# Kernel tuning notes

Measured on AMD Instinct MI355X. Metric: run time of the kernel, lower is better.

Reference implementation:

```python
import jax, jax.numpy as jnp
from jax import lax
import numpy as np

T, B, D, H = 4096, 32, 512, 256


def setup_inputs() -> dict:
    key = jax.random.key(0)
    ks = jax.random.split(key, 8)
    s_ih = 1.0 / np.sqrt(H)
    inp = {
        "x": jax.random.normal(ks[0], (T, B, D), dtype=jnp.float32),
        "reset": jax.random.randint(ks[1], (T, B), 0, 2, dtype=jnp.int32),
        # PyTorch nn.LSTM params, gate order (i, f, g, o)
        "W_ih": jax.random.uniform(ks[2], (4 * H, D), jnp.float32, -s_ih, s_ih),
        "W_hh": jax.random.uniform(ks[3], (4 * H, H), jnp.float32, -s_ih, s_ih),
        "b_ih": jax.random.uniform(ks[4], (4 * H,), jnp.float32, -s_ih, s_ih),
        "b_hh": jax.random.uniform(ks[5], (4 * H,), jnp.float32, -s_ih, s_ih),
        "W_proj": jax.random.uniform(ks[6], (1, H), jnp.float32, -s_ih, s_ih),
        "b_proj": jax.random.uniform(ks[7], (1,), jnp.float32, -s_ih, s_ih),
    }
    return inp


def _lstm_with_reset(x, reset, W_ih, W_hh, b_ih, b_hh):
    # Precompute input contribution for all timesteps: [T, B, 4H]
    xW = jnp.einsum("tbd,gd->tbg", x, W_ih) + b_ih + b_hh
    h0 = jnp.zeros((x.shape[1], H), x.dtype)
    c0 = jnp.zeros((x.shape[1], H), x.dtype)

    def step(carry, inp):
        h, c = carry
        xw, r = inp
        keep = (1 - r).astype(h.dtype)[:, None]  # zero state at episode starts
        h = h * keep
        c = c * keep
        gates = xw + h @ W_hh.T  # [B, 4H]
        i, f, g, o = jnp.split(gates, 4, axis=-1)
        c = jax.nn.sigmoid(f) * c + jax.nn.sigmoid(i) * jnp.tanh(g)
        h = jax.nn.sigmoid(o) * jnp.tanh(c)
        return (h, c), h

    (_, _), hs = lax.scan(step, (h0, c0), (xW, reset))
    return hs  # [T, B, H]


def reference(x, reset, W_ih, W_hh, b_ih, b_hh, W_proj, b_proj):
    hs = _lstm_with_reset(x, reset, W_ih, W_hh, b_ih, b_hh)
    return hs @ W_proj.T + b_proj  # [T, B, 1]
```

## Files before the change

kernel.cpp:

```cpp
#include <hip/hip_runtime.h>
#include <cstdint>
#include <cstddef>

#define T_DIM 4096
#define B_DIM 32
#define D_DIM 512
#define H_DIM 256
#define G_DIM 1024
#define HSTR 264
#define NBUCK 64

typedef _Float16 h8 __attribute__((ext_vector_type(8)));
typedef float f4 __attribute__((ext_vector_type(4)));

__global__ void seg_build_kernel(const int* __restrict__ reset,
                                 unsigned* __restrict__ starts,
                                 unsigned* __restrict__ segcnt) {
  __shared__ unsigned cnts[256];
  __shared__ unsigned offs[256];
  const int b = blockIdx.x;
  const int tid = threadIdx.x;
  const int t0 = tid * 16;
  unsigned c = 0;
  for (int e = 0; e < 16; ++e) {
    int t = t0 + e;
    bool pred = (t == 0) || (reset[t * B_DIM + b] != 0);
    c += pred ? 1u : 0u;
  }
  cnts[tid] = c;
  __syncthreads();
  if (tid == 0) {
    unsigned run = 0;
    for (int i = 0; i < 256; ++i) { unsigned v = cnts[i]; offs[i] = run; run += v; }
    segcnt[b] = run;
  }
  __syncthreads();
  unsigned o = (unsigned)b * 4096u + offs[tid];
  for (int e = 0; e < 16; ++e) {
    int t = t0 + e;
    bool pred = (t == 0) || (reset[t * B_DIM + b] != 0);
    if (pred) { starts[o++] = (unsigned)t; }
  }
}

__global__ void seg_flat_kernel(const unsigned* __restrict__ starts,
                                const unsigned* __restrict__ segcnt,
                                uint2* __restrict__ flat2,
                                unsigned* __restrict__ meta) {
  __shared__ unsigned offs;
  const int b = blockIdx.x;
  const int tid = threadIdx.x;
  if (tid == 0) {
    unsigned o = 0;
    for (int i = 0; i < b; ++i) o += segcnt[i];
    offs = o;
    if (b == 31) meta[1] = o + segcnt[31];
    if (b == 0) meta[0] = 0u;
  }
  __syncthreads();
  const unsigned cnt = segcnt[b];
  const unsigned off = offs;
  for (unsigned s = tid; s < cnt; s += 256) {
    unsigned t0 = starts[b * 4096u + s];
    unsigned t1 = (s + 1 < cnt) ? starts[b * 4096u + s + 1] : 4096u;
    flat2[off + s] = make_uint2(t0 | ((unsigned)b << 16), t1);
  }
}

__global__ void seg_sort_kernel(const uint2* __restrict__ flat2,
                                uint2* __restrict__ flat,
                                const unsigned* __restrict__ meta) {
  __shared__ unsigned lh[NBUCK];
  __shared__ unsigned cur[NBUCK];
  const unsigned nseg = meta[1];
  const int tid = threadIdx.x;
  const int lane = tid & 63;
  if (tid < NBUCK) lh[tid] = 0u;
  __syncthreads();
  for (unsigned base = 0; base < nseg; base += 1024) {
    unsigned i = base + tid;
    bool act = i < nseg;
    unsigned bk = 0u;
    if (act) {
      uint2 e = flat2[i];
      bk = min(e.y - (e.x & 0xFFFFu), (unsigned)NBUCK) - 1u;
    }
    unsigned long long rem = __ballot(act);
    while (rem) {
      int ld = (int)__ffsll((unsigned long long)rem) - 1;
      unsigned lbk = __shfl(bk, ld);
      unsigned long long meq = __ballot(act && bk == lbk);
      if (lane == ld) atomicAdd(&lh[lbk], (unsigned)__popcll(meq));
      rem &= ~meq;
    }
  }
  __syncthreads();
  if (tid == 0) {
    unsigned run = 0;
    for (int k = NBUCK - 1; k >= 0; --k) { cur[k] = run; run += lh[k]; }
  }
  __syncthreads();
  for (unsigned base = 0; base < nseg; base += 1024) {
    unsigned i = base + tid;
    bool act = i < nseg;
    uint2 e = make_uint2(0u, 0u);
    unsigned bk = 0u;
    if (act) {
      e = flat2[i];
      bk = min(e.y - (e.x & 0xFFFFu), (unsigned)NBUCK) - 1u;
    }
    unsigned long long rem = __ballot(act);
    unsigned pos = 0u;
    while (rem) {
      int ld = (int)__ffsll((unsigned long long)rem) - 1;
      unsigned lbk = __shfl(bk, ld);
      unsigned long long meq = __ballot(act && bk == lbk);
      unsigned bs = 0u;
      if (lane == ld) bs = atomicAdd(&cur[lbk], (unsigned)__popcll(meq));
      bs = __shfl(bs, ld);
      if (act && bk == lbk)
        pos = bs + (unsigned)__popcll(meq & ((1ull << lane) - 1ull));
      rem &= ~meq;
    }
    if (act) flat[pos] = e;
  }
}

__global__ void wpack_kernel(const float* __restrict__ Whh,
                             _Float16* __restrict__ wpack) {
  int gid = blockIdx.x * 256 + threadIdx.x;
  int nt = gid >> 9;
  int rem = gid & 511;
  int ks = rem >> 6;
  int l = rem & 63;
  int n = nt * 16 + (l & 15);
  int k = ks * 32 + (l >> 4) * 8;
  const float* src = Whh + (size_t)n * H_DIM + k;
  f4 v0 = *(const f4*)src;
  f4 v1 = *(const f4*)(src + 4);
  h8 wv = {(_Float16)v0.x, (_Float16)v0.y, (_Float16)v0.z, (_Float16)v0.w,
           (_Float16)v1.x, (_Float16)v1.y, (_Float16)v1.z, (_Float16)v1.w};
  *(h8*)(wpack + (size_t)gid * 8) = wv;
}

#define BM 128
#define BN 128
#define BK 32

__global__ __launch_bounds__(256) void xw_gemm_kernel(
    const float* __restrict__ X, const float* __restrict__ Wih,
    const float* __restrict__ bih, const float* __restrict__ bhh,
    _Float16* __restrict__ xw) {
  __shared__ _Float16 As[BM * BK];
  __shared__ _Float16 Bs[BN * BK];
  const int tid = threadIdx.x;
  const int lane = tid & 63;
  const int wave = tid >> 6;
  const unsigned wg = blockIdx.x;
  const unsigned xcd = wg & 7u;
  const unsigned idx = wg >> 3;
  const size_t m0 = (size_t)(xcd * 128u + (idx >> 3)) * BM;
  const int n0 = (int)(idx & 7u) * BN;
  const int wm = (wave & 1) * 64;
  const int wn = (wave >> 1) * 64;
  const int q = lane >> 4;
  const int r = lane & 15;

  f4 acc[4][4];
#pragma unroll
  for (int i = 0; i < 4; ++i)
#pragma unroll
    for (int j = 0; j < 4; ++j) { f4 z = {0.f, 0.f, 0.f, 0.f}; acc[i][j] = z; }

  const int srow = tid >> 1;
  const int kh = (tid & 1) * 16;

  for (int k0 = 0; k0 < D_DIM; k0 += BK) {
    const float* ax = X + (m0 + (size_t)srow) * D_DIM + k0 + kh;
    const float* bx = Wih + ((size_t)(n0 + srow)) * D_DIM + k0 + kh;
    f4 a0 = *(const f4*)(ax);
    f4 a1 = *(const f4*)(ax + 4);
    f4 a2 = *(const f4*)(ax + 8);
    f4 a3 = *(const f4*)(ax + 12);
    f4 b0 = *(const f4*)(bx);
    f4 b1 = *(const f4*)(bx + 4);
    f4 b2 = *(const f4*)(bx + 8);
    f4 b3 = *(const f4*)(bx + 12);
    h8 ha0 = {(_Float16)a0.x, (_Float16)a0.y, (_Float16)a0.z, (_Float16)a0.w,
              (_Float16)a1.x, (_Float16)a1.y, (_Float16)a1.z, (_Float16)a1.w};
    h8 ha1 = {(_Float16)a2.x, (_Float16)a2.y, (_Float16)a2.z, (_Float16)a2.w,
              (_Float16)a3.x, (_Float16)a3.y, (_Float16)a3.z, (_Float16)a3.w};
    h8 hb0 = {(_Float16)b0.x, (_Float16)b0.y, (_Float16)b0.z, (_Float16)b0.w,
              (_Float16)b1.x, (_Float16)b1.y, (_Float16)b1.z, (_Float16)b1.w};
    h8 hb1 = {(_Float16)b2.x, (_Float16)b2.y, (_Float16)b2.z, (_Float16)b2.w,
              (_Float16)b3.x, (_Float16)b3.y, (_Float16)b3.z, (_Float16)b3.w};
    *(h8*)(As + srow * BK + kh) = ha0;
    *(h8*)(As + srow * BK + kh + 8) = ha1;
    *(h8*)(Bs + srow * BK + kh) = hb0;
    *(h8*)(Bs + srow * BK + kh + 8) = hb1;
    __syncthreads();

    h8 af[4], bf[4];
#pragma unroll
    for (int mi = 0; mi < 4; ++mi)
      af[mi] = *(const h8*)(As + (wm + mi * 16 + r) * BK + q * 8);
#pragma unroll
    for (int ni = 0; ni < 4; ++ni)
      bf[ni] = *(const h8*)(Bs + (wn + ni * 16 + r) * BK + q * 8);
#pragma unroll
    for (int mi = 0; mi < 4; ++mi)
#pragma unroll
      for (int ni = 0; ni < 4; ++ni)
        acc[mi][ni] = __builtin_amdgcn_mfma_f32_16x16x32_f16(af[mi], bf[ni], acc[mi][ni], 0, 0, 0);
    __syncthreads();
  }

#pragma unroll
  for (int mi = 0; mi < 4; ++mi) {
#pragma unroll
    for (int ni = 0; ni < 4; ++ni) {
      int n = n0 + wn + ni * 16 + r;
      float bias = bih[n] + bhh[n];
#pragma unroll
      for (int reg = 0; reg < 4; ++reg) {
        size_t m = m0 + (size_t)(wm + mi * 16 + q * 4 + reg);
        __builtin_nontemporal_store((_Float16)(acc[mi][ni][reg] + bias),
                                    &xw[m * G_DIM + n]);
      }
    }
  }
}

__device__ __forceinline__ float sigmf(float x) {
  return __builtin_amdgcn_rcpf(1.f + __expf(-x));
}
__device__ __forceinline__ float tanhf_(float x) {
  return 2.f * __builtin_amdgcn_rcpf(1.f + __expf(-2.f * x)) - 1.f;
}
__device__ __forceinline__ f4 MF(h8 a, h8 b, f4 c) {
  return __builtin_amdgcn_mfma_f32_16x16x32_f16(a, b, c, 0, 0, 0);
}

#define WPKp(g, j, ks) \
  ((const h8*)(wpack + (((size_t)((((g)*16 + 2*w + (j)) * 8 + (ks))) * 64 + l) * 8)))
#define WLDp(g, j, ks2) \
  (*(const h8*)(Wlds + ((((ks2)*64) + ((g)*16 + 2*w + (j))) * 64 + l) * 8))
#define ARD(mt, ks) (*(const h8*)(Hbuf + (16*(mt) + r16) * HSTR + (ks)*32 + q*8))

#define MFK_REG(KS) do {                                                   \
  h8 a0_ = ARD(0, KS), a1_ = ARD(1, KS);                                   \
  _Pragma("unroll") for (int g = 0; g < 4; ++g)                            \
  _Pragma("unroll") for (int j = 0; j < 2; ++j) {                          \
    acc[0][g][j] = MF(a0_, wr[g][j][KS], acc[0][g][j]);                    \
    acc[1][g][j] = MF(a1_, wr[g][j][KS], acc[1][g][j]); }                  \
} while (0)

#define MFK_LDS(KS2, KS) do {                                              \
  h8 a0_ = ARD(0, KS), a1_ = ARD(1, KS);                                   \
  _Pragma("unroll") for (int g = 0; g < 4; ++g)                            \
  _Pragma("unroll") for (int j = 0; j < 2; ++j) {                          \
    h8 b_ = WLDp(g, j, KS2);                                               \
    acc[0][g][j] = MF(a0_, b_, acc[0][g][j]);                              \
    acc[1][g][j] = MF(a1_, b_, acc[1][g][j]); }                            \
} while (0)

#define MFK_STR(KS) do {                                                   \
  h8 a0_ = ARD(0, KS), a1_ = ARD(1, KS);                                   \
  _Pragma("unroll") for (int g = 0; g < 4; ++g)                            \
  _Pragma("unroll") for (int j = 0; j < 2; ++j) {                          \
    acc[0][g][j] = MF(a0_, sreg[g][j], acc[0][g][j]);                      \
    acc[1][g][j] = MF(a1_, sreg[g][j], acc[1][g][j]); }                    \
} while (0)

#define LOAD_STR(KS) do {                                                  \
  _Pragma("unroll") for (int g = 0; g < 4; ++g)                            \
  _Pragma("unroll") for (int j = 0; j < 2; ++j)                            \
    sreg[g][j] = *WPKp(g, j, KS);                                          \
} while (0)

#define XWG(MT, G, J, RB, NB) do {                                         \
  f4 xv;                                                                   \
  xv.x = (float)__builtin_nontemporal_load(                                \
      (const _Float16*)(xwc + RB.x + (G)*512 + (NB)));                     \
  xv.y = (float)__builtin_nontemporal_load(                                \
      (const _Float16*)(xwc + RB.y + (G)*512 + (NB)));                     \
  xv.z = (float)__builtin_nontemporal_load(                                \
      (const _Float16*)(xwc + RB.z + (G)*512 + (NB)));                     \
  xv.w = (float)__builtin_nontemporal_load(                                \
      (const _Float16*)(xwc + RB.w + (G)*512 + (NB)));                     \
  acc[MT][G][J] += xv; } while (0)

#define CONTROL_STEP do {                                                    \
  int m = tid;                                                               \
  if (alivef[m]) {                                                           \
    unsigned oi = outix[m];                                                  \
    if (oi != 0xFFFFFFFFu) {                                                 \
      float s = bp;                                                          \
      _Pragma("unroll") for (int ww = 0; ww < 8; ++ww) s += pbuf[ww][m];     \
      __builtin_nontemporal_store(s, &out[oi]);                              \
    }                                                                        \
    int t = tcur[m] + 1;                                                     \
    if (t < tend[m]) {                                                       \
      tcur[m] = t; keepm[m] = 1.f;                                           \
      unsigned row = (unsigned)t * 32u + (unsigned)bcol[m];                  \
      trowB[m] = row * 2048u; outix[m] = row;                                \
    } else {                                                                 \
      unsigned idx = atomicAdd(ctr, 1u);                                     \
      if (idx < nseg) {                                                      \
        uint2 sg = flat[idx];                                                \
        int t0s = (int)(sg.x & 0xFFFFu); int bb = (int)(sg.x >> 16);         \
        tcur[m] = t0s; tend[m] = (int)sg.y; bcol[m] = bb; keepm[m] = 0.f;    \
        unsigned row = (unsigned)t0s * 32u + (unsigned)bb;                   \
        trowB[m] = row * 2048u; outix[m] = row;                              \
        h8 zz = {0,0,0,0,0,0,0,0};                                           \
        _Pragma("unroll") for (int i2 = 0; i2 < 33; ++i2)                    \
          *(h8*)(Hbuf + (size_t)m * HSTR + i2 * 8) = zz;                     \
      } else {                                                               \
        alivef[m] = 0; outix[m] = 0xFFFFFFFFu; trowB[m] = 0;                 \
        keepm[m] = 0.f;                                                      \
      }                                                                      \
    }                                                                        \
  }                                                                          \
} while (0)

__global__ __launch_bounds__(512, 2) void lstm_scan_mfma(
    const _Float16* __restrict__ xw,
    const _Float16* __restrict__ wpack,
    const float* __restrict__ Wproj,
    const float* __restrict__ bproj,
    const uint2* __restrict__ flat,
    unsigned* __restrict__ meta,
    float* __restrict__ out) {
  __shared__ __align__(16) _Float16 Wlds[2 * 64 * 64 * 8];
  __shared__ __align__(16) _Float16 Hbuf[32 * HSTR];
  __shared__ __align__(16) float pbuf[8][32];
  __shared__ __align__(16) unsigned trowB[32];
  __shared__ __align__(16) float keepm[32];
  __shared__ unsigned outix[32];
  __shared__ int tcur[32], tend[32], bcol[32], alivef[32];

  const int tid = threadIdx.x;
  const int l = tid & 63;
  const int w = tid >> 6;
  const int q = l >> 4;
  const int r16 = l & 15;
  const char* xwc = (const char*)xw;
  unsigned* ctr = meta;
  const unsigned nseg = meta[1];

  for (int it = 0; it < 16; ++it) {
    int idx = it * 512 + tid;
    int ks2 = idx >> 12;
    int nt = (idx >> 6) & 63;
    int ll = idx & 63;
    *(h8*)(Wlds + (size_t)idx * 8) =
        *(const h8*)(wpack + (((size_t)(nt * 8 + ks2 + 4)) * 64 + ll) * 8);
  }
  for (int i = tid; i < 32 * HSTR / 8; i += 512) {
    h8 z = {0,0,0,0,0,0,0,0};
    *(h8*)(Hbuf + (size_t)i * 8) = z;
  }
  h8 wr[4][2][4];
#pragma unroll
  for (int g = 0; g < 4; ++g)
#pragma unroll
    for (int j = 0; j < 2; ++j)
#pragma unroll
      for (int ks = 0; ks < 4; ++ks)
        wr[g][j][ks] = *WPKp(g, j, ks);

  const float wpv0 = Wproj[32 * w + r16];
  const float wpv1 = Wproj[32 * w + 16 + r16];
  const float bp = bproj[0];
  if (tid < 32) {
    alivef[tid] = 1; tcur[tid] = 0; tend[tid] = 0; bcol[tid] = 0;
    outix[tid] = 0xFFFFFFFFu; trowB[tid] = 0; keepm[tid] = 0.f;
  }
  float cst[16];
#pragma unroll
  for (int i = 0; i < 16; ++i) cst[i] = 0.f;
  __syncthreads();
  if (tid < 32) CONTROL_STEP;
  int nalive = __syncthreads_count(tid < 32 ? alivef[tid] : 0);

  while (nalive > 0) {
    f4 z4 = {0.f, 0.f, 0.f, 0.f};
    f4 acc[2][4][2];
#pragma unroll
    for (int mt = 0; mt < 2; ++mt)
#pragma unroll
      for (int g = 0; g < 4; ++g)
#pragma unroll
        for (int j = 0; j < 2; ++j) acc[mt][g][j] = z4;
    h8 sreg[4][2];

    LOAD_STR(6);
    MFK_REG(0);
    MFK_STR(6);
    LOAD_STR(7);
    MFK_REG(1);
    MFK_STR(7);
    MFK_REG(2);
    MFK_REG(3);
    MFK_LDS(0, 4);
    MFK_LDS(1, 5);

    __syncthreads();

    uint4 rb0 = *(const uint4*)&trowB[q * 4];
    uint4 rb1 = *(const uint4*)&trowB[16 + q * 4];
    const int nb0 = w * 64 + r16 * 2;
    const int nb1 = nb0 + 32;
    XWG(0, 0, 0, rb0, nb0); XWG(0, 0, 1, rb0, nb1);
    XWG(0, 1, 0, rb0, nb0); XWG(0, 1, 1, rb0, nb1);
    XWG(0, 2, 0, rb0, nb0); XWG(0, 2, 1, rb0, nb1);
    XWG(0, 3, 0, rb0, nb0); XWG(0, 3, 1, rb0, nb1);
    XWG(1, 0, 0, rb1, nb0); XWG(1, 0, 1, rb1, nb1);
    XWG(1, 1, 0, rb1, nb0); XWG(1, 1, 1, rb1, nb1);
    XWG(1, 2, 0, rb1, nb0); XWG(1, 2, 1, rb1, nb1);
    XWG(1, 3, 0, rb1, nb0); XWG(1, 3, 1, rb1, nb1);

    f4 kp0 = *(const f4*)&keepm[q * 4];
    f4 kp1 = *(const f4*)&keepm[16 + q * 4];
    float pr[8];
#pragma unroll
    for (int r = 0; r < 4; ++r) {
      {
        float gi = sigmf(acc[0][0][0][r]);
        float gf = sigmf(acc[0][1][0][r]);
        float gg = tanhf_(acc[0][2][0][r]);
        float go = sigmf(acc[0][3][0][r]);
        float cn = gf * (cst[r] * kp0[r]) + gi * gg;
        cst[r] = cn;
        float hv = go * tanhf_(cn);
        Hbuf[(q * 4 + r) * HSTR + 32 * w + r16] = (_Float16)hv;
        pr[r] = hv * wpv0;
      }
      {
        float gi = sigmf(acc[0][0][1][r]);
        float gf = sigmf(acc[0][1][1][r]);
        float gg = tanhf_(acc[0][2][1][r]);
        float go = sigmf(acc[0][3][1][r]);
        float cn = gf * (cst[4 + r] * kp0[r]) + gi * gg;
        cst[4 + r] = cn;
        float hv = go * tanhf_(cn);
        Hbuf[(q * 4 + r) * HSTR + 32 * w + 16 + r16] = (_Float16)hv;
        pr[r] += hv * wpv1;
      }
    }
#pragma unroll
    for (int r = 0; r < 4; ++r) {
      {
        float gi = sigmf(acc[1][0][0][r]);
        float gf = sigmf(acc[1][1][0][r]);
        float gg = tanhf_(acc[1][2][0][r]);
        float go = sigmf(acc[1][3][0][r]);
        float cn = gf * (cst[8 + r] * kp1[r]) + gi * gg;
        cst[8 + r] = cn;
        float hv = go * tanhf_(cn);
        Hbuf[(16 + q * 4 + r) * HSTR + 32 * w + r16] = (_Float16)hv;
        pr[4 + r] = hv * wpv0;
      }
      {
        float gi = sigmf(acc[1][0][1][r]);
        float gf = sigmf(acc[1][1][1][r]);
        float gg = tanhf_(acc[1][2][1][r]);
        float go = sigmf(acc[1][3][1][r]);
        float cn = gf * (cst[12 + r] * kp1[r]) + gi * gg;
        cst[12 + r] = cn;
        float hv = go * tanhf_(cn);
        Hbuf[(16 + q * 4 + r) * HSTR + 32 * w + 16 + r16] = (_Float16)hv;
        pr[4 + r] += hv * wpv1;
      }
    }
#pragma unroll
    for (int jj = 0; jj < 8; ++jj) {
      pr[jj] += __shfl_xor(pr[jj], 1);
      pr[jj] += __shfl_xor(pr[jj], 2);
      pr[jj] += __shfl_xor(pr[jj], 4);
      pr[jj] += __shfl_xor(pr[jj], 8);
    }
    if (r16 == 0) {
#pragma unroll
      for (int jj = 0; jj < 8; ++jj)
        pbuf[w][16 * (jj >> 2) + q * 4 + (jj & 3)] = pr[jj];
    }

    __syncthreads();
    if (tid < 32) CONTROL_STEP;
    nalive = __syncthreads_count(tid < 32 ? alivef[tid] : 0);
  }
}

extern "C" void kernel_launch(void* const* d_in, const int* in_sizes, int n_in,
                              void* d_out, int out_size, void* d_ws, size_t ws_size,
                              hipStream_t stream) {
  const float* x = (const float*)d_in[0];
  const int* reset = (const int*)d_in[1];
  const float* Wih = (const float*)d_in[2];
  const float* Whh = (const float*)d_in[3];
  const float* bih = (const float*)d_in[4];
  const float* bhh = (const float*)d_in[5];
  const float* Wproj = (const float*)d_in[6];
  const float* bproj = (const float*)d_in[7];
  float* out = (float*)d_out;

  char* ws = (char*)d_ws;
  _Float16* xw = (_Float16*)ws;
  unsigned* starts = (unsigned*)(ws + 268435456ULL);
  unsigned* segcnt = (unsigned*)(ws + 268959744ULL);
  uint2* flat = (uint2*)(ws + 268959872ULL);
  _Float16* wpack = (_Float16*)(ws + 270008448ULL);
  unsigned* meta = (unsigned*)(ws + 270532736ULL);
  uint2* flat2 = (uint2*)ws;

  hipLaunchKernelGGL(seg_build_kernel, dim3(32), dim3(256), 0, stream,
                     reset, starts, segcnt);
  hipLaunchKernelGGL(seg_flat_kernel, dim3(32), dim3(256), 0, stream,
                     starts, segcnt, flat2, meta);
  hipLaunchKernelGGL(seg_sort_kernel, dim3(1), dim3(1024), 0, stream,
                     flat2, flat, meta);
  hipLaunchKernelGGL(wpack_kernel, dim3(128), dim3(256), 0, stream,
                     Whh, wpack);
  hipLaunchKernelGGL(xw_gemm_kernel, dim3(8192), dim3(256), 0, stream,
                     x, Wih, bih, bhh, xw);
  hipLaunchKernelGGL(lstm_scan_mfma, dim3(256), dim3(512), 0, stream,
                     xw, wpack, Wproj, bproj, flat, meta, out);
}
```

Measured before the change: 1.276 ms.

## Stage xW rows into LDS via async global_load_lds and rebalance W_hh placement

At the start of each recurrent step, the 32 rows of precomputed input gates are prefetched into an LDS buffer with async global-to-LDS loads, which overlap the recurrent MFMA work. Previously each lane issued many scattered nontemporal fp16 global loads after the barrier. The W_hh k-slices are redistributed: fewer are held in registers, one is held in LDS, and the rest are streamed from global memory through double-buffered registers. The segment-claim atomic is aggregated per wavefront with a ballot, and the GEMM store becomes a normal store so xW stays in cache. The cost is extra LDS, which may limit occupancy, and more global weight traffic per step.

```diff
diff --git a/kernel.cpp b/kernel.cpp
--- a/kernel.cpp
+++ b/kernel.cpp
@@ -8,6 +8,7 @@
 #define H_DIM 256
 #define G_DIM 1024
 #define HSTR 264
+#define XSTR 1036
 #define NBUCK 64
 
 typedef _Float16 h8 __attribute__((ext_vector_type(8)));
@@ -224,8 +225,7 @@
 #pragma unroll
       for (int reg = 0; reg < 4; ++reg) {
         size_t m = m0 + (size_t)(wm + mi * 16 + q * 4 + reg);
-        __builtin_nontemporal_store((_Float16)(acc[mi][ni][reg] + bias),
-                                    &xw[m * G_DIM + n]);
+        xw[m * G_DIM + n] = (_Float16)(acc[mi][ni][reg] + bias);
       }
     }
   }
@@ -243,8 +243,6 @@
 
 #define WPKp(g, j, ks) \
   ((const h8*)(wpack + (((size_t)((((g)*16 + 2*w + (j)) * 8 + (ks))) * 64 + l) * 8)))
-#define WLDp(g, j, ks2) \
-  (*(const h8*)(Wlds + ((((ks2)*64) + ((g)*16 + 2*w + (j))) * 64 + l) * 8))
 #define ARD(mt, ks) (*(const h8*)(Hbuf + (16*(mt) + r16) * HSTR + (ks)*32 + q*8))
 
 #define MFK_REG(KS) do {                                                   \
@@ -255,72 +253,83 @@
     acc[1][g][j] = MF(a1_, wr[g][j][KS], acc[1][g][j]); }                  \
 } while (0)
 
-#define MFK_LDS(KS2, KS) do {                                              \
+#define MFK_W2() do {                                                      \
+  h8 a0_ = ARD(0, 2), a1_ = ARD(1, 2);                                     \
+  _Pragma("unroll") for (int g = 0; g < 4; ++g)                            \
+  _Pragma("unroll") for (int j = 0; j < 2; ++j) {                          \
+    h8 b_ = *(const h8*)(Wlds + (size_t)((((g)*16 + 2*w + (j)) * 64 + l)) * 8); \
+    acc[0][g][j] = MF(a0_, b_, acc[0][g][j]);                              \
+    acc[1][g][j] = MF(a1_, b_, acc[1][g][j]); }                            \
+} while (0)
+
+#define MFK_S(BUF, KS) do {                                                \
   h8 a0_ = ARD(0, KS), a1_ = ARD(1, KS);                                   \
   _Pragma("unroll") for (int g = 0; g < 4; ++g)                            \
   _Pragma("unroll") for (int j = 0; j < 2; ++j) {                          \
-    h8 b_ = WLDp(g, j, KS2);                                               \
-    acc[0][g][j] = MF(a0_, b_, acc[0][g][j]);                              \
-    acc[1][g][j] = MF(a1_, b_, acc[1][g][j]); }                            \
+    acc[0][g][j] = MF(a0_, BUF[g][j], acc[0][g][j]);                       \
+    acc[1][g][j] = MF(a1_, BUF[g][j], acc[1][g][j]); }                     \
 } while (0)
 
-#define MFK_STR(KS) do {                                                   \
-  h8 a0_ = ARD(0, KS), a1_ = ARD(1, KS);                                   \
-  _Pragma("unroll") for (int g = 0; g < 4; ++g)                            \
-  _Pragma("unroll") for (int j = 0; j < 2; ++j) {                          \
-    acc[0][g][j] = MF(a0_, sreg[g][j], acc[0][g][j]);                      \
-    acc[1][g][j] = MF(a1_, sreg[g][j], acc[1][g][j]); }                    \
-} while (0)
-
-#define LOAD_STR(KS) do {                                                  \
+#define LOAD_S(BUF, KS) do {                                               \
   _Pragma("unroll") for (int g = 0; g < 4; ++g)                            \
   _Pragma("unroll") for (int j = 0; j < 2; ++j)                            \
-    sreg[g][j] = *WPKp(g, j, KS);                                          \
+    BUF[g][j] = *WPKp(g, j, KS);                                           \
 } while (0)
 
-#define XWG(MT, G, J, RB, NB) do {                                         \
+#define XRD(MT, G, J) do {                                                 \
   f4 xv;                                                                   \
-  xv.x = (float)__builtin_nontemporal_load(                                \
-      (const _Float16*)(xwc + RB.x + (G)*512 + (NB)));                     \
-  xv.y = (float)__builtin_nontemporal_load(                                \
-      (const _Float16*)(xwc + RB.y + (G)*512 + (NB)));                     \
-  xv.z = (float)__builtin_nontemporal_load(                                \
-      (const _Float16*)(xwc + RB.z + (G)*512 + (NB)));                     \
-  xv.w = (float)__builtin_nontemporal_load(                                \
-      (const _Float16*)(xwc + RB.w + (G)*512 + (NB)));                     \
+  int rb_ = 16*(MT) + q*4;                                                 \
+  int nn_ = (G)*256 + w*32 + 16*(J) + r16;                                 \
+  xv.x = (float)xwlds[(rb_+0)*XSTR + nn_];                                 \
+  xv.y = (float)xwlds[(rb_+1)*XSTR + nn_];                                 \
+  xv.z = (float)xwlds[(rb_+2)*XSTR + nn_];                                 \
+  xv.w = (float)xwlds[(rb_+3)*XSTR + nn_];                                 \
   acc[MT][G][J] += xv; } while (0)
 
-#define CONTROL_STEP do {                                                    \
-  int m = tid;                                                               \
-  if (alivef[m]) {                                                           \
-    unsigned oi = outix[m];                                                  \
-    if (oi != 0xFFFFFFFFu) {                                                 \
-      float s = bp;                                                          \
-      _Pragma("unroll") for (int ww = 0; ww < 8; ++ww) s += pbuf[ww][m];     \
-      __builtin_nontemporal_store(s, &out[oi]);                              \
-    }                                                                        \
-    int t = tcur[m] + 1;                                                     \
-    if (t < tend[m]) {                                                       \
-      tcur[m] = t; keepm[m] = 1.f;                                           \
-      unsigned row = (unsigned)t * 32u + (unsigned)bcol[m];                  \
-      trowB[m] = row * 2048u; outix[m] = row;                                \
-    } else {                                                                 \
-      unsigned idx = atomicAdd(ctr, 1u);                                     \
-      if (idx < nseg) {                                                      \
-        uint2 sg = flat[idx];                                                \
-        int t0s = (int)(sg.x & 0xFFFFu); int bb = (int)(sg.x >> 16);         \
-        tcur[m] = t0s; tend[m] = (int)sg.y; bcol[m] = bb; keepm[m] = 0.f;    \
-        unsigned row = (unsigned)t0s * 32u + (unsigned)bb;                   \
-        trowB[m] = row * 2048u; outix[m] = row;                              \
-        h8 zz = {0,0,0,0,0,0,0,0};                                           \
-        _Pragma("unroll") for (int i2 = 0; i2 < 33; ++i2)                    \
-          *(h8*)(Hbuf + (size_t)m * HSTR + i2 * 8) = zz;                     \
-      } else {                                                               \
-        alivef[m] = 0; outix[m] = 0xFFFFFFFFu; trowB[m] = 0;                 \
-        keepm[m] = 0.f;                                                      \
-      }                                                                      \
-    }                                                                        \
-  }                                                                          \
+#define CONTROL_STEP do {                                                     \
+  int m = tid;                                                                \
+  bool aliv = alivef[m] != 0;                                                 \
+  if (aliv) {                                                                 \
+    unsigned oi = outix[m];                                                   \
+    if (oi != 0xFFFFFFFFu) {                                                  \
+      float s = bp;                                                           \
+      _Pragma("unroll") for (int ww = 0; ww < 8; ++ww) s += pbuf[ww][m];      \
+      __builtin_nontemporal_store(s, &out[oi]);                               \
+    }                                                                         \
+  }                                                                           \
+  bool cont = aliv && (tcur[m] + 1 < tend[m]);                                \
+  bool need = aliv && !cont;                                                  \
+  unsigned long long bal = __ballot(need);                                    \
+  if (cont) {                                                                 \
+    int t = tcur[m] + 1;                                                      \
+    tcur[m] = t; keepm[m] = 1.f;                                              \
+    unsigned row = (unsigned)t * 32u + (unsigned)bcol[m];                     \
+    trowB[m] = row * 2048u; outix[m] = row;                                   \
+  }                                                                           \
+  if (bal) {                                                                  \
+    unsigned cntp = (unsigned)__popcll(bal);                                  \
+    int ldr = (int)__ffsll(bal) - 1;                                          \
+    unsigned basep = 0;                                                       \
+    if ((tid & 63) == ldr) basep = atomicAdd(ctr, cntp);                      \
+    basep = __shfl(basep, ldr);                                               \
+    if (need) {                                                               \
+      unsigned idx = basep +                                                  \
+          (unsigned)__popcll(bal & ((1ull << (tid & 63)) - 1ull));            \
+      if (idx < nseg) {                                                       \
+        uint2 sg = flat[idx];                                                 \
+        int t0s = (int)(sg.x & 0xFFFFu); int bb = (int)(sg.x >> 16);          \
+        tcur[m] = t0s; tend[m] = (int)sg.y; bcol[m] = bb; keepm[m] = 0.f;     \
+        unsigned row = (unsigned)t0s * 32u + (unsigned)bb;                    \
+        trowB[m] = row * 2048u; outix[m] = row;                               \
+        h8 zz = {0,0,0,0,0,0,0,0};                                            \
+        _Pragma("unroll") for (int i2 = 0; i2 < 33; ++i2)                     \
+          *(h8*)(Hbuf + (size_t)m * HSTR + i2 * 8) = zz;                      \
+      } else {                                                                \
+        alivef[m] = 0; outix[m] = 0xFFFFFFFFu; trowB[m] = 0;                  \
+        keepm[m] = 0.f;                                                       \
+      }                                                                       \
+    }                                                                         \
+  }                                                                           \
 } while (0)
 
 __global__ __launch_bounds__(512, 2) void lstm_scan_mfma(
@@ -331,7 +340,8 @@
     const uint2* __restrict__ flat,
     unsigned* __restrict__ meta,
     float* __restrict__ out) {
-  __shared__ __align__(16) _Float16 Wlds[2 * 64 * 64 * 8];
+  __shared__ __align__(16) _Float16 Wlds[64 * 64 * 8];
+  __shared__ __align__(16) _Float16 xwlds[32 * XSTR];
   __shared__ __align__(16) _Float16 Hbuf[32 * HSTR];
   __shared__ __align__(16) float pbuf[8][32];
   __shared__ __align__(16) unsigned trowB[32];
@@ -350,23 +360,22 @@
 
   for (int it = 0; it < 16; ++it) {
     int idx = it * 512 + tid;
-    int ks2 = idx >> 12;
-    int nt = (idx >> 6) & 63;
+    int nt = idx >> 6;
     int ll = idx & 63;
     *(h8*)(Wlds + (size_t)idx * 8) =
-        *(const h8*)(wpack + (((size_t)(nt * 8 + ks2 + 4)) * 64 + ll) * 8);
+        *(const h8*)(wpack + (((size_t)(nt * 8 + 2)) * 64 + ll) * 8);
   }
   for (int i = tid; i < 32 * HSTR / 8; i += 512) {
     h8 z = {0,0,0,0,0,0,0,0};
     *(h8*)(Hbuf + (size_t)i * 8) = z;
   }
-  h8 wr[4][2][4];
+  h8 wr[4][2][2];
 #pragma unroll
   for (int g = 0; g < 4; ++g)
 #pragma unroll
     for (int j = 0; j < 2; ++j)
 #pragma unroll
-      for (int ks = 0; ks < 4; ++ks)
+      for (int ks = 0; ks < 2; ++ks)
         wr[g][j][ks] = *WPKp(g, j, ks);
 
   const float wpv0 = Wproj[32 * w + r16];
@@ -384,6 +393,15 @@
   int nalive = __syncthreads_count(tid < 32 ? alivef[tid] : 0);
 
   while (nalive > 0) {
+#pragma unroll
+    for (int rnd = 0; rnd < 8; ++rnd) {
+      int c = rnd * 8 + w;
+      unsigned rowB = trowB[c >> 1];
+      const char* src = xwc + (size_t)rowB + (size_t)((c & 1) * 1024) + (size_t)l * 16;
+      _Float16* dst = xwlds + (size_t)(c >> 1) * XSTR + (c & 1) * 512;
+      __builtin_amdgcn_global_load_lds((const uint32_t*)src, (uint32_t*)dst, 16, 0, 0);
+    }
+
     f4 z4 = {0.f, 0.f, 0.f, 0.f};
     f4 acc[2][4][2];
 #pragma unroll
@@ -392,33 +410,28 @@
       for (int g = 0; g < 4; ++g)
 #pragma unroll
         for (int j = 0; j < 2; ++j) acc[mt][g][j] = z4;
-    h8 sreg[4][2];
-
-    LOAD_STR(6);
+    h8 sA[4][2], sB[4][2];
+
+    LOAD_S(sA, 3); LOAD_S(sB, 4);
     MFK_REG(0);
-    MFK_STR(6);
-    LOAD_STR(7);
     MFK_REG(1);
-    MFK_STR(7);
-    MFK_REG(2);
-    MFK_REG(3);
-    MFK_LDS(0, 4);
-    MFK_LDS(1, 5);
+    MFK_W2();
+    MFK_S(sA, 3); LOAD_S(sA, 5);
+    MFK_S(sB, 4); LOAD_S(sB, 6);
+    MFK_S(sA, 5); LOAD_S(sA, 7);
+    MFK_S(sB, 6);
+    MFK_S(sA, 7);
 
     __syncthreads();
 
-    uint4 rb0 = *(const uint4*)&trowB[q * 4];
-    uint4 rb1 = *(const uint4*)&trowB[16 + q * 4];
-    const int nb0 = w * 64 + r16 * 2;
-    const int nb1 = nb0 + 32;
-    XWG(0, 0, 0, rb0, nb0); XWG(0, 0, 1, rb0, nb1);
-    XWG(0, 1, 0, rb0, nb0); XWG(0, 1, 1, rb0, nb1);
-    XWG(0, 2, 0, rb0, nb0); XWG(0, 2, 1, rb0, nb1);
-    XWG(0, 3, 0, rb0, nb0); XWG(0, 3, 1, rb0, nb1);
-    XWG(1, 0, 0, rb1, nb0); XWG(1, 0, 1, rb1, nb1);
-    XWG(1, 1, 0, rb1, nb0); XWG(1, 1, 1, rb1, nb1);
-    XWG(1, 2, 0, rb1, nb0); XWG(1, 2, 1, rb1, nb1);
-    XWG(1, 3, 0, rb1, nb0); XWG(1, 3, 1, rb1, nb1);
+    XRD(0, 0, 0); XRD(0, 0, 1);
+    XRD(0, 1, 0); XRD(0, 1, 1);
+    XRD(0, 2, 0); XRD(0, 2, 1);
+    XRD(0, 3, 0); XRD(0, 3, 1);
+    XRD(1, 0, 0); XRD(1, 0, 1);
+    XRD(1, 1, 0); XRD(1, 1, 1);
+    XRD(1, 2, 0); XRD(1, 2, 1);
+    XRD(1, 3, 0); XRD(1, 3, 1);
 
     f4 kp0 = *(const f4*)&keepm[q * 4];
     f4 kp1 = *(const f4*)&keepm[16 + q * 4];
```

New measurement: 1.207 ms. -5.4%, faster.
